# Performance work log

Hardware: AMD Instinct MI355X
Metric: run time of the kernel (lower is better)

The kernel has to match this reference:

```python
import jax, jax.numpy as jnp
import numpy as np

N_NODES = 100000
N_EDGES = 1600000
HID = 150
N_LAYERS = 5


def setup_inputs() -> dict:
    key = jax.random.key(0)
    ks = jax.random.split(key, 7)
    s = 1.0 / np.sqrt(HID)
    return {
        "x": jax.random.normal(ks[0], (N_NODES, HID), dtype=jnp.float32),
        "weight": jax.random.uniform(ks[1], (N_LAYERS, HID, HID), jnp.float32, -s, s),
        "w_ih": jax.random.uniform(ks[2], (3 * HID, HID), jnp.float32, -s, s),
        "w_hh": jax.random.uniform(ks[3], (3 * HID, HID), jnp.float32, -s, s),
        "b_ih": jax.random.uniform(ks[4], (3 * HID,), jnp.float32, -s, s),
        "b_hh": jax.random.uniform(ks[5], (3 * HID,), jnp.float32, -s, s),
        "edge_index": jax.random.randint(ks[6], (2, N_EDGES), 0, N_NODES, dtype=jnp.int32),
    }


def _gru_cell(inp, h, w_ih, w_hh, b_ih, b_hh):
    # torch.nn.GRUCell math
    gi = inp @ w_ih.T + b_ih            # [N, 3H]
    gh = h @ w_hh.T + b_hh              # [N, 3H]
    i_r, i_z, i_n = jnp.split(gi, 3, axis=-1)
    h_r, h_z, h_n = jnp.split(gh, 3, axis=-1)
    r = jax.nn.sigmoid(i_r + h_r)
    z = jax.nn.sigmoid(i_z + h_z)
    n = jnp.tanh(i_n + r * h_n)
    return (1.0 - z) * n + z * h


def reference(x, weight, w_ih, w_hh, b_ih, b_hh, edge_index):
    # GatedGraphConv: h'_i = GRU( sum_{j->i} (h_j @ W_l), h_i ), repeated num_layers times
    src, dst = edge_index[0], edge_index[1]
    n_nodes = x.shape[0]
    h = x
    for l in range(weight.shape[0]):
        m = h @ weight[l]                                        # [N, H] transform
        aggr = jax.ops.segment_sum(m[src], dst, num_segments=n_nodes)  # scatter-add over edges
        h = _gru_cell(aggr, h, w_ih, w_hh, b_ih, b_hh)
    return h
```

## Files before the change

kernel.cpp:

```cpp
#include <hip/hip_runtime.h>
#include <hip/hip_bf16.h>
#include <cmath>

#define HID 150
#define NN 100000
#define NE 1600000
#define NL 5
#define G3 (3*HID)
#define KP 320
#define NP 640
#define KS 10
#define BM 64
#define HSTEPS 20
#define HS_BF (20*64*8)

#define NPBSH 9
#define NBK 196
#define CAPL 64
#define CAPG 10240
#define CHUNK 4096
#define BPAD 16

typedef __hip_bfloat16 bf16;
using short8 = __attribute__((ext_vector_type(8))) short;
using f32x4  = __attribute__((ext_vector_type(4))) float;

static __device__ __forceinline__ unsigned short bf_bits(float v) {
    __hip_bfloat16 h = __float2bfloat16(v);
    return *reinterpret_cast<unsigned short*>(&h);
}

static __device__ __forceinline__ float blo(unsigned int p) {
    return __uint_as_float((p & 0xffffu) << 16);
}
static __device__ __forceinline__ float bhi(unsigned int p) {
    return __uint_as_float(p & 0xffff0000u);
}

static __device__ __forceinline__ void gld_lds16(const void* g, void* l) {
    __builtin_amdgcn_global_load_lds(
        (const __attribute__((address_space(1))) void*)g,
        (__attribute__((address_space(3))) void*)l, 16, 0, 0);
}

__global__ void build_wfrag(const float* __restrict__ W, const float* __restrict__ w_ih,
                            const float* __restrict__ w_hh, const float* __restrict__ b_ih,
                            const float* __restrict__ b_hh, bf16* __restrict__ wfrag) {
    int idx = blockIdx.x * 256 + threadIdx.x;
    if (idx >= NL * KP * NP) return;
    int j = idx % NP;
    int k = (idx / NP) % KP;
    int l = idx / (NP * KP);
    int sec = j / 160;
    int f = j - sec * 160;
    float v = 0.f;
    if (f < HID) {
        if (k < HID) {
            if (sec < 3) {
                const float* Wl = W + (size_t)l * HID * HID + (size_t)k * HID;
                const float* wr = w_ih + (size_t)(sec * HID + f) * HID;
                float acc = 0.f;
                for (int t = 0; t < HID; ++t) acc += Wl[t] * wr[t];
                v = acc;
            }
        } else if (k == HID) {
            v = (sec == 0) ? b_ih[f] + b_hh[f]
              : (sec == 1) ? b_ih[HID + f] + b_hh[HID + f]
              : (sec == 2) ? b_ih[2 * HID + f]
                           : b_hh[2 * HID + f];
        } else if (k >= 160 && k < 160 + HID) {
            int kk = k - 160;
            if (sec == 0)      v = w_hh[(size_t)f * HID + kk];
            else if (sec == 1) v = w_hh[(size_t)(HID + f) * HID + kk];
            else if (sec == 3) v = w_hh[(size_t)(2 * HID + f) * HID + kk];
        }
    }
    int kstep = k >> 5, kq = (k >> 3) & 3, ki = k & 7;
    int half = sec >> 1, s2 = sec & 1;
    int fgroup = f >> 4, nl = j & 15;
    int tl = s2 * 10 + fgroup;
    int lane = kq * 16 + nl;
    size_t addr = ((((size_t)(l * KS + kstep) * 2 + half) * 20 + tl) * 64 + lane) * 8 + ki;
    wfrag[addr] = __float2bfloat16(v);
}

__global__ __launch_bounds__(256)
void bin_edges(const int* __restrict__ ei, int* __restrict__ bcnt,
               unsigned int* __restrict__ bbuf) {
    __shared__ int lcnt[NBK];
    __shared__ unsigned int lstage[NBK * CAPL];
    int t = threadIdx.x;
    for (int i = t; i < NBK; i += 256) lcnt[i] = 0;
    __syncthreads();
    int e0 = blockIdx.x * CHUNK;
#pragma unroll
    for (int it = 0; it < CHUNK / 256; ++it) {
        int e = e0 + it * 256 + t;
        if (e < NE) {
            int src = ei[e], dst = ei[NE + e];
            int b = dst >> NPBSH;
            unsigned int v = (unsigned int)src | ((unsigned int)(dst & 511) << 17);
            int li = atomicAdd(&lcnt[b], 1);
            if (li < CAPL) {
                lstage[b * CAPL + li] = v;
            } else {
                int gp = atomicAdd(&bcnt[b * BPAD], 1);
                if (gp < CAPG) bbuf[(size_t)b * CAPG + gp] = v;
            }
        }
    }
    __syncthreads();
    int wave = t >> 6, lane = t & 63;
    for (int b = wave; b < NBK; b += 4) {
        int cnt = lcnt[b];
        if (cnt > CAPL) cnt = CAPL;
        if (cnt == 0) continue;
        int base = 0;
        if (lane == 0) base = atomicAdd(&bcnt[b * BPAD], cnt);
        base = __shfl(base, 0, 64);
        if (lane < cnt && base + lane < CAPG)
            bbuf[(size_t)b * CAPG + base + lane] = lstage[b * CAPL + lane];
    }
}

__global__ __launch_bounds__(256)
void csr_from_buckets(const int* __restrict__ bcnt, const unsigned int* __restrict__ bbuf,
                      int* __restrict__ off, int* __restrict__ csr) {
    __shared__ int hist[512];
    __shared__ int s[256];
    int b = blockIdx.x, t = threadIdx.x;
    hist[t] = 0;
    hist[256 + t] = 0;
    int base = 0;
    for (int i = 0; i < b; ++i) {
        int c = bcnt[i * BPAD];
        base += (c > CAPG) ? CAPG : c;
    }
    int cnt = bcnt[b * BPAD];
    if (cnt > CAPG) cnt = CAPG;
    __syncthreads();
    for (int i = t; i < cnt; i += 256) {
        unsigned int v = bbuf[(size_t)b * CAPG + i];
        atomicAdd(&hist[v >> 17], 1);
    }
    __syncthreads();
    int a0 = hist[2 * t], a1 = hist[2 * t + 1];
    int tsum = a0 + a1;
    s[t] = tsum;
    __syncthreads();
    for (int d = 1; d < 256; d <<= 1) {
        int u = (t >= d) ? s[t - d] : 0;
        __syncthreads();
        s[t] += u;
        __syncthreads();
    }
    int tb = base + s[t] - tsum;
    hist[2 * t] = tb;
    hist[2 * t + 1] = tb + a0;
    int node = (b << NPBSH) + 2 * t;
    if (node < NN) off[node] = tb;
    if (node + 1 < NN) off[node + 1] = tb + a0;
    if (b == NBK - 1 && t == 255) off[NN] = base + s[255];
    __syncthreads();
    for (int i = t; i < cnt; i += 256) {
        unsigned int v = bbuf[(size_t)b * CAPG + i];
        int p = atomicAdd(&hist[v >> 17], 1);
        csr[p] = (int)(v & 0x1FFFFu);
    }
}

__global__ void init_h(const float* __restrict__ x, bf16* __restrict__ Abuf) {
    size_t i = (size_t)blockIdx.x * 256 + threadIdx.x;
    if (i >= (size_t)NN * HID) return;
    int m = (int)(i / HID), f = (int)(i - (size_t)m * HID);
    Abuf[(size_t)m * KP + 160 + f] = __float2bfloat16(x[i]);
}

__global__ __launch_bounds__(256)
void aggregate(bf16* __restrict__ Abuf, const int* __restrict__ off,
               const int* __restrict__ csr) {
    int node = (blockIdx.x * blockDim.x + threadIdx.x) >> 6;
    int lane = threadIdx.x & 63;
    if (node >= NN) return;
    int e0 = off[node], e1 = off[node + 1];
    float a0 = 0.f, a1 = 0.f, b0 = 0.f, b1 = 0.f;
    bool tail = lane < 11;
    int e = e0;
    for (; e + 8 <= e1; e += 8) {
        const unsigned int* r0 = (const unsigned int*)(Abuf + (size_t)csr[e]     * KP + 160);
        const unsigned int* r1 = (const unsigned int*)(Abuf + (size_t)csr[e + 1] * KP + 160);
        const unsigned int* r2 = (const unsigned int*)(Abuf + (size_t)csr[e + 2] * KP + 160);
        const unsigned int* r3 = (const unsigned int*)(Abuf + (size_t)csr[e + 3] * KP + 160);
        const unsigned int* r4 = (const unsigned int*)(Abuf + (size_t)csr[e + 4] * KP + 160);
        const unsigned int* r5 = (const unsigned int*)(Abuf + (size_t)csr[e + 5] * KP + 160);
        const unsigned int* r6 = (const unsigned int*)(Abuf + (size_t)csr[e + 6] * KP + 160);
        const unsigned int* r7 = (const unsigned int*)(Abuf + (size_t)csr[e + 7] * KP + 160);
        unsigned int p0 = r0[lane], p1 = r1[lane], p2 = r2[lane], p3 = r3[lane];
        unsigned int p4 = r4[lane], p5 = r5[lane], p6 = r6[lane], p7 = r7[lane];
        unsigned int q0 = 0, q1 = 0, q2 = 0, q3 = 0, q4 = 0, q5 = 0, q6 = 0, q7 = 0;
        if (tail) {
            q0 = r0[64 + lane]; q1 = r1[64 + lane]; q2 = r2[64 + lane]; q3 = r3[64 + lane];
            q4 = r4[64 + lane]; q5 = r5[64 + lane]; q6 = r6[64 + lane]; q7 = r7[64 + lane];
        }
        a0 += blo(p0) + blo(p1) + blo(p2) + blo(p3) + blo(p4) + blo(p5) + blo(p6) + blo(p7);
        a1 += bhi(p0) + bhi(p1) + bhi(p2) + bhi(p3) + bhi(p4) + bhi(p5) + bhi(p6) + bhi(p7);
        b0 += blo(q0) + blo(q1) + blo(q2) + blo(q3) + blo(q4) + blo(q5) + blo(q6) + blo(q7);
        b1 += bhi(q0) + bhi(q1) + bhi(q2) + bhi(q3) + bhi(q4) + bhi(q5) + bhi(q6) + bhi(q7);
    }
    for (; e + 4 <= e1; e += 4) {
        const unsigned int* r0 = (const unsigned int*)(Abuf + (size_t)csr[e]     * KP + 160);
        const unsigned int* r1 = (const unsigned int*)(Abuf + (size_t)csr[e + 1] * KP + 160);
        const unsigned int* r2 = (const unsigned int*)(Abuf + (size_t)csr[e + 2] * KP + 160);
        const unsigned int* r3 = (const unsigned int*)(Abuf + (size_t)csr[e + 3] * KP + 160);
        unsigned int p0 = r0[lane], p1 = r1[lane], p2 = r2[lane], p3 = r3[lane];
        unsigned int q0 = 0, q1 = 0, q2 = 0, q3 = 0;
        if (tail) { q0 = r0[64 + lane]; q1 = r1[64 + lane]; q2 = r2[64 + lane]; q3 = r3[64 + lane]; }
        a0 += blo(p0) + blo(p1) + blo(p2) + blo(p3);
        a1 += bhi(p0) + bhi(p1) + bhi(p2) + bhi(p3);
        b0 += blo(q0) + blo(q1) + blo(q2) + blo(q3);
        b1 += bhi(q0) + bhi(q1) + bhi(q2) + bhi(q3);
    }
    for (; e < e1; ++e) {
        const unsigned int* r = (const unsigned int*)(Abuf + (size_t)csr[e] * KP + 160);
        unsigned int p = r[lane];
        unsigned int q = tail ? r[64 + lane] : 0;
        a0 += blo(p); a1 += bhi(p);
        b0 += blo(q); b1 += bhi(q);
    }
    unsigned int* out = (unsigned int*)(Abuf + (size_t)node * KP);
    out[lane] = (unsigned int)bf_bits(a0) | ((unsigned int)bf_bits(a1) << 16);
    if (tail) out[64 + lane] = (unsigned int)bf_bits(b0) | ((unsigned int)bf_bits(b1) << 16);
    if (lane < 5) out[75 + lane] = (lane == 0) ? 0x00003F80u : 0u;
}

__global__ __launch_bounds__(256, 2)
void gemm_gru(const bf16* __restrict__ Abuf, const bf16* __restrict__ wfrag_l,
              float* __restrict__ h_out, bf16* __restrict__ Abuf_w, int last) {
    __shared__ __align__(16) bf16 Bs[3][HS_BF];
    __shared__ __align__(16) bf16 As3[3][BM * 32];
    int tid = threadIdx.x;
    int wave = tid >> 6, lane = tid & 63;
    int mh = wave >> 1, nh = wave & 1;
    int row0 = blockIdx.x * BM;

    const char* gbase = (const char*)(Abuf + (size_t)row0 * KP);
    int ar = tid >> 2, aq = tid & 3;

    auto stageB = [&](int hs) {
        const char* gb = (const char*)(wfrag_l + (size_t)hs * HS_BF);
        char* lb = (char*)Bs[hs % 3];
#pragma unroll
        for (int it = 0; it < 5; ++it) {
            int c = it * 256 + tid;
            gld_lds16(gb + (size_t)c * 16, lb + (size_t)c * 16);
        }
    };
    auto stageA = [&](int ks) {
        gld_lds16(gbase + (size_t)ar * (KP * 2) + ks * 64 + aq * 16,
                  (char*)As3[ks % 3] + (size_t)tid * 16);
    };

    stageB(0); stageA(0); stageB(1); stageA(1);

    f32x4 acc[2][20];
#pragma unroll
    for (int mt = 0; mt < 2; ++mt)
#pragma unroll
        for (int t = 0; t < 20; ++t) acc[mt][t] = (f32x4){0.f, 0.f, 0.f, 0.f};

    int col = lane & 15, q = lane >> 4;
    short8 a0, a1;
#pragma unroll
    for (int hs = 0; hs < HSTEPS; ++hs) {
        if (hs < 18)       asm volatile("s_waitcnt vmcnt(6)" ::: "memory");
        else if (hs == 18) asm volatile("s_waitcnt vmcnt(5)" ::: "memory");
        else               asm volatile("s_waitcnt vmcnt(0)" ::: "memory");
        __builtin_amdgcn_s_barrier();
        __builtin_amdgcn_sched_barrier(0);

        int ks = hs >> 1, half = hs & 1, cur = hs % 3;
        if (half == 0) {
            const bf16* Ak = As3[ks % 3];
            a0 = *(const short8*)(Ak + ((mh * 32 + col) * 32 + q * 8));
            a1 = *(const short8*)(Ak + ((mh * 32 + 16 + col) * 32 + q * 8));
        }
#pragma unroll
        for (int g = 0; g < 5; ++g) {
#pragma unroll
            for (int s2 = 0; s2 < 2; ++s2) {
                int tl = s2 * 10 + nh * 5 + g;
                short8 b = *(const short8*)(Bs[cur] + ((size_t)(tl * 64 + lane) * 8));
                int t = g * 4 + half * 2 + s2;
                acc[0][t] = __builtin_amdgcn_mfma_f32_16x16x32_bf16(a0, b, acc[0][t], 0, 0, 0);
                acc[1][t] = __builtin_amdgcn_mfma_f32_16x16x32_bf16(a1, b, acc[1][t], 0, 0, 0);
            }
        }
        if (hs + 2 < HSTEPS) stageB(hs + 2);
        if (half == 1 && ks + 2 < KS) stageA(ks + 2);
    }

    int qrow = q * 4;
    bf16* Cs = &Bs[0][0];
#pragma unroll
    for (int mt = 0; mt < 2; ++mt) {
#pragma unroll
        for (int g = 0; g < 5; ++g) {
            int f = (nh * 5 + g) * 16 + col;
            if (f < HID) {
                f32x4 ar4 = acc[mt][g * 4 + 0], az = acc[mt][g * 4 + 1];
                f32x4 an = acc[mt][g * 4 + 2], ah = acc[mt][g * 4 + 3];
#pragma unroll
                for (int v = 0; v < 4; ++v) {
                    int rl = mh * 32 + mt * 16 + qrow + v;
                    float hp = __bfloat162float(Abuf[(size_t)(row0 + rl) * KP + 160 + f]);
                    float r = 1.f / (1.f + __expf(-ar4[v]));
                    float z = 1.f / (1.f + __expf(-az[v]));
                    float n = tanhf(an[v] + r * ah[v]);
                    float ho = (1.f - z) * n + z * hp;
                    if (last) {
                        int m = row0 + rl;
                        if (m < NN) h_out[(size_t)m * HID + f] = ho;
                    } else {
                        Cs[rl * 160 + f] = __float2bfloat16(ho);
                    }
                }
            }
        }
    }
    if (!last) {
        __syncthreads();
        const unsigned int* src = (const unsigned int*)Cs;
        for (int i = tid; i < 64 * 75; i += 256) {
            int r = i / 75, dw = i - r * 75;
            ((unsigned int*)(Abuf_w + (size_t)(row0 + r) * KP + 160))[dw] =
                src[r * 80 + dw];
        }
    }
}

extern "C" void kernel_launch(void* const* d_in, const int* in_sizes, int n_in,
                              void* d_out, int out_size, void* d_ws, size_t ws_size,
                              hipStream_t stream) {
    const float* x      = (const float*)d_in[0];
    const float* weight = (const float*)d_in[1];
    const float* w_ih   = (const float*)d_in[2];
    const float* w_hh   = (const float*)d_in[3];
    const float* b_ih   = (const float*)d_in[4];
    const float* b_hh   = (const float*)d_in[5];
    const int*   ei     = (const int*)d_in[6];
    float* h = (float*)d_out;

    const int nblk = (NN + BM - 1) / BM;
    const size_t NNP = (size_t)nblk * BM;
    char* p = (char*)d_ws;
    auto alloc = [&](size_t bytes) { char* r = p; p += (bytes + 255) & ~255ull; return r; };
    int*  off   = (int*)alloc((size_t)(NN + 1) * 4);
    int*  csr   = (int*)alloc((size_t)NE * 4);
    int*  bcnt  = (int*)alloc((size_t)NBK * BPAD * 4);
    unsigned int* bbuf = (unsigned int*)alloc((size_t)NBK * CAPG * 4);
    bf16* wfrag = (bf16*)alloc((size_t)NL * KS * 2 * HS_BF * 2);
    bf16* Abuf  = (bf16*)alloc((NNP + BM) * (size_t)KP * 2);

    hipMemsetAsync(bcnt, 0, (size_t)NBK * BPAD * 4, stream);
    build_wfrag<<<(NL * KP * NP + 255) / 256, 256, 0, stream>>>(weight, w_ih, w_hh, b_ih, b_hh, wfrag);
    bin_edges<<<(NE + CHUNK - 1) / CHUNK, 256, 0, stream>>>(ei, bcnt, bbuf);
    csr_from_buckets<<<NBK, 256, 0, stream>>>(bcnt, bbuf, off, csr);
    init_h<<<(int)(((size_t)NN * HID + 255) / 256), 256, 0, stream>>>(x, Abuf);

    for (int l = 0; l < NL; ++l) {
        aggregate<<<(NN * 64 + 255) / 256, 256, 0, stream>>>(Abuf, off, csr);
        gemm_gru<<<nblk, 256, 0, stream>>>(Abuf, wfrag + (size_t)l * KS * 2 * HS_BF,
                                           h, Abuf, (l == NL - 1) ? 1 : 0);
    }
}
```

Baseline: 1.100 ms.

## Double GEMM row tile and load A fragments directly from global

The fused GEMM+GRU kernel now processes 128 rows per block with 512 threads instead of 64 rows with 256. A operands are read straight from global memory into registers rather than staged through LDS. The weight tile is shared by more rows, which cuts redundant B staging per output row, and the B staging moves to 4-byte global-to-LDS loads issued before the MFMAs. The launch bounds now request 4 blocks of 512 threads per CU, which caps each thread at about 64 VGPRs, while the accumulators need 160 floats per thread. That risks heavy register spilling. Direct A loads also expose global latency in the MFMA loop without prefetch.

```diff
diff --git a/kernel.cpp b/kernel.cpp
--- a/kernel.cpp
+++ b/kernel.cpp
@@ -10,7 +10,7 @@
 #define KP 320
 #define NP 640
 #define KS 10
-#define BM 64
+#define BM 128
 #define HSTEPS 20
 #define HS_BF (20*64*8)
 
@@ -41,6 +41,12 @@
     __builtin_amdgcn_global_load_lds(
         (const __attribute__((address_space(1))) void*)g,
         (__attribute__((address_space(3))) void*)l, 16, 0, 0);
+}
+
+static __device__ __forceinline__ void gld_lds4(const void* g, void* l) {
+    __builtin_amdgcn_global_load_lds(
+        (const __attribute__((address_space(1))) void*)g,
+        (__attribute__((address_space(3))) void*)l, 4, 0, 0);
 }
 
 __global__ void build_wfrag(const float* __restrict__ W, const float* __restrict__ w_ih,
@@ -233,34 +239,32 @@
     if (lane < 5) out[75 + lane] = (lane == 0) ? 0x00003F80u : 0u;
 }
 
-__global__ __launch_bounds__(256, 2)
+__global__ __launch_bounds__(512, 4)
 void gemm_gru(const bf16* __restrict__ Abuf, const bf16* __restrict__ wfrag_l,
               float* __restrict__ h_out, bf16* __restrict__ Abuf_w, int last) {
     __shared__ __align__(16) bf16 Bs[3][HS_BF];
-    __shared__ __align__(16) bf16 As3[3][BM * 32];
     int tid = threadIdx.x;
     int wave = tid >> 6, lane = tid & 63;
     int mh = wave >> 1, nh = wave & 1;
     int row0 = blockIdx.x * BM;
 
-    const char* gbase = (const char*)(Abuf + (size_t)row0 * KP);
-    int ar = tid >> 2, aq = tid & 3;
+    int col = lane & 15, q = lane >> 4;
+    const char* abase0 = (const char*)Abuf
+        + (size_t)(row0 + mh * 32 + col) * (KP * 2) + q * 16;
+    const char* abase1 = abase0 + 16 * (KP * 2);
 
     auto stageB = [&](int hs) {
         const char* gb = (const char*)(wfrag_l + (size_t)hs * HS_BF);
         char* lb = (char*)Bs[hs % 3];
 #pragma unroll
-        for (int it = 0; it < 5; ++it) {
-            int c = it * 256 + tid;
-            gld_lds16(gb + (size_t)c * 16, lb + (size_t)c * 16);
+        for (int it = 0; it < 10; ++it) {
+            int c = it * 512 + tid;
+            gld_lds4(gb + (size_t)c * 4, lb + (size_t)c * 4);
         }
     };
-    auto stageA = [&](int ks) {
-        gld_lds16(gbase + (size_t)ar * (KP * 2) + ks * 64 + aq * 16,
-                  (char*)As3[ks % 3] + (size_t)tid * 16);
-    };
-
-    stageB(0); stageA(0); stageB(1); stageA(1);
+
+    stageB(0);
+    stageB(1);
 
     f32x4 acc[2][20];
 #pragma unroll
@@ -268,22 +272,21 @@
 #pragma unroll
         for (int t = 0; t < 20; ++t) acc[mt][t] = (f32x4){0.f, 0.f, 0.f, 0.f};
 
-    int col = lane & 15, q = lane >> 4;
     short8 a0, a1;
 #pragma unroll
     for (int hs = 0; hs < HSTEPS; ++hs) {
-        if (hs < 18)       asm volatile("s_waitcnt vmcnt(6)" ::: "memory");
-        else if (hs == 18) asm volatile("s_waitcnt vmcnt(5)" ::: "memory");
-        else               asm volatile("s_waitcnt vmcnt(0)" ::: "memory");
+        if (hs < 19) asm volatile("s_waitcnt vmcnt(10)" ::: "memory");
+        else         asm volatile("s_waitcnt vmcnt(0)" ::: "memory");
         __builtin_amdgcn_s_barrier();
         __builtin_amdgcn_sched_barrier(0);
 
         int ks = hs >> 1, half = hs & 1, cur = hs % 3;
         if (half == 0) {
-            const bf16* Ak = As3[ks % 3];
-            a0 = *(const short8*)(Ak + ((mh * 32 + col) * 32 + q * 8));
-            a1 = *(const short8*)(Ak + ((mh * 32 + 16 + col) * 32 + q * 8));
-        }
+            a0 = *(const short8*)(abase0 + ks * 64);
+            a1 = *(const short8*)(abase1 + ks * 64);
+            __builtin_amdgcn_sched_barrier(0);
+        }
+        if (hs + 2 < HSTEPS) stageB(hs + 2);
 #pragma unroll
         for (int g = 0; g < 5; ++g) {
 #pragma unroll
@@ -295,9 +298,9 @@
                 acc[1][t] = __builtin_amdgcn_mfma_f32_16x16x32_bf16(a1, b, acc[1][t], 0, 0, 0);
             }
         }
-        if (hs + 2 < HSTEPS) stageB(hs + 2);
-        if (half == 1 && ks + 2 < KS) stageA(ks + 2);
-    }
+    }
+
+    __syncthreads();
 
     int qrow = q * 4;
     bf16* Cs = &Bs[0][0];
@@ -330,10 +333,10 @@
     if (!last) {
         __syncthreads();
         const unsigned int* src = (const unsigned int*)Cs;
-        for (int i = tid; i < 64 * 75; i += 256) {
-            int r = i / 75, dw = i - r * 75;
-            ((unsigned int*)(Abuf_w + (size_t)(row0 + r) * KP + 160))[dw] =
-                src[r * 80 + dw];
+        for (int i = tid; i < 128 * 75; i += 512) {
+            int r2 = i / 75, dw = i - r2 * 75;
+            ((unsigned int*)(Abuf_w + (size_t)(row0 + r2) * KP + 160))[dw] =
+                src[r2 * 80 + dw];
         }
     }
 }
@@ -369,7 +372,7 @@
 
     for (int l = 0; l < NL; ++l) {
         aggregate<<<(NN * 64 + 255) / 256, 256, 0, stream>>>(Abuf, off, csr);
-        gemm_gru<<<nblk, 256, 0, stream>>>(Abuf, wfrag + (size_t)l * KS * 2 * HS_BF,
+        gemm_gru<<<nblk, 512, 0, stream>>>(Abuf, wfrag + (size_t)l * KS * 2 * HS_BF,
                                            h, Abuf, (l == NL - 1) ? 1 : 0);
     }
 }
```

New measurement: 3.365 ms. 3.06x slower.

## Load GEMM operands directly from global into registers, dropping LDS staging pipeline

Applied to the files above, without the earlier changes.

Removes the triple-buffered global_load_lds staging of weight fragments and A tiles along with its waitcnt/barrier pipeline. Each wave now loads its B fragments and A rows straight from global memory (relying on cache) into registers before issuing the MFMAs, and LDS holds only the output staging tile. Launch bounds no longer request two blocks per CU and the loop is unrolled by two instead of fully. The aim is to shed barrier and LDS overhead, at the cost of exposed global latency and redundant weight reads across waves and blocks.

```diff
diff --git a/kernel.cpp b/kernel.cpp
--- a/kernel.cpp
+++ b/kernel.cpp
@@ -35,12 +35,6 @@
 }
 static __device__ __forceinline__ float bhi(unsigned int p) {
     return __uint_as_float(p & 0xffff0000u);
-}
-
-static __device__ __forceinline__ void gld_lds16(const void* g, void* l) {
-    __builtin_amdgcn_global_load_lds(
-        (const __attribute__((address_space(1))) void*)g,
-        (__attribute__((address_space(3))) void*)l, 16, 0, 0);
 }
 
 __global__ void build_wfrag(const float* __restrict__ W, const float* __restrict__ w_ih,
@@ -233,34 +227,19 @@
     if (lane < 5) out[75 + lane] = (lane == 0) ? 0x00003F80u : 0u;
 }
 
-__global__ __launch_bounds__(256, 2)
+__global__ __launch_bounds__(256)
 void gemm_gru(const bf16* __restrict__ Abuf, const bf16* __restrict__ wfrag_l,
               float* __restrict__ h_out, bf16* __restrict__ Abuf_w, int last) {
-    __shared__ __align__(16) bf16 Bs[3][HS_BF];
-    __shared__ __align__(16) bf16 As3[3][BM * 32];
+    __shared__ __align__(16) bf16 Cs[64 * 160];
     int tid = threadIdx.x;
     int wave = tid >> 6, lane = tid & 63;
     int mh = wave >> 1, nh = wave & 1;
     int row0 = blockIdx.x * BM;
 
-    const char* gbase = (const char*)(Abuf + (size_t)row0 * KP);
-    int ar = tid >> 2, aq = tid & 3;
-
-    auto stageB = [&](int hs) {
-        const char* gb = (const char*)(wfrag_l + (size_t)hs * HS_BF);
-        char* lb = (char*)Bs[hs % 3];
-#pragma unroll
-        for (int it = 0; it < 5; ++it) {
-            int c = it * 256 + tid;
-            gld_lds16(gb + (size_t)c * 16, lb + (size_t)c * 16);
-        }
-    };
-    auto stageA = [&](int ks) {
-        gld_lds16(gbase + (size_t)ar * (KP * 2) + ks * 64 + aq * 16,
-                  (char*)As3[ks % 3] + (size_t)tid * 16);
-    };
-
-    stageB(0); stageA(0); stageB(1); stageA(1);
+    int col = lane & 15, q = lane >> 4;
+    const char* abase0 = (const char*)Abuf
+        + (size_t)(row0 + mh * 32 + col) * (KP * 2) + q * 16;
+    const char* abase1 = abase0 + 16 * (KP * 2);
 
     f32x4 acc[2][20];
 #pragma unroll
@@ -268,39 +247,36 @@
 #pragma unroll
         for (int t = 0; t < 20; ++t) acc[mt][t] = (f32x4){0.f, 0.f, 0.f, 0.f};
 
-    int col = lane & 15, q = lane >> 4;
     short8 a0, a1;
-#pragma unroll
+#pragma unroll 2
     for (int hs = 0; hs < HSTEPS; ++hs) {
-        if (hs < 18)       asm volatile("s_waitcnt vmcnt(6)" ::: "memory");
-        else if (hs == 18) asm volatile("s_waitcnt vmcnt(5)" ::: "memory");
-        else               asm volatile("s_waitcnt vmcnt(0)" ::: "memory");
-        __builtin_amdgcn_s_barrier();
-        __builtin_amdgcn_sched_barrier(0);
-
-        int ks = hs >> 1, half = hs & 1, cur = hs % 3;
-        if (half == 0) {
-            const bf16* Ak = As3[ks % 3];
-            a0 = *(const short8*)(Ak + ((mh * 32 + col) * 32 + q * 8));
-            a1 = *(const short8*)(Ak + ((mh * 32 + 16 + col) * 32 + q * 8));
-        }
+        int ks = hs >> 1, half = hs & 1;
+        const bf16* wf = wfrag_l + (size_t)hs * HS_BF;
+        short8 bf[10];
 #pragma unroll
         for (int g = 0; g < 5; ++g) {
 #pragma unroll
             for (int s2 = 0; s2 < 2; ++s2) {
                 int tl = s2 * 10 + nh * 5 + g;
-                short8 b = *(const short8*)(Bs[cur] + ((size_t)(tl * 64 + lane) * 8));
+                bf[g * 2 + s2] = *(const short8*)(wf + (size_t)(tl * 64 + lane) * 8);
+            }
+        }
+        if (half == 0) {
+            a0 = *(const short8*)(abase0 + ks * 64);
+            a1 = *(const short8*)(abase1 + ks * 64);
+        }
+#pragma unroll
+        for (int g = 0; g < 5; ++g) {
+#pragma unroll
+            for (int s2 = 0; s2 < 2; ++s2) {
                 int t = g * 4 + half * 2 + s2;
-                acc[0][t] = __builtin_amdgcn_mfma_f32_16x16x32_bf16(a0, b, acc[0][t], 0, 0, 0);
-                acc[1][t] = __builtin_amdgcn_mfma_f32_16x16x32_bf16(a1, b, acc[1][t], 0, 0, 0);
-            }
-        }
-        if (hs + 2 < HSTEPS) stageB(hs + 2);
-        if (half == 1 && ks + 2 < KS) stageA(ks + 2);
+                acc[0][t] = __builtin_amdgcn_mfma_f32_16x16x32_bf16(a0, bf[g * 2 + s2], acc[0][t], 0, 0, 0);
+                acc[1][t] = __builtin_amdgcn_mfma_f32_16x16x32_bf16(a1, bf[g * 2 + s2], acc[1][t], 0, 0, 0);
+            }
+        }
     }
 
     int qrow = q * 4;
-    bf16* Cs = &Bs[0][0];
 #pragma unroll
     for (int mt = 0; mt < 2; ++mt) {
 #pragma unroll
```

After: 1.443 ms. 1.31x slower.
